# Performance work log

Hardware: AMD Instinct MI355X
Metric: run time of the kernel (lower is better)

The kernel has to match this reference:

```python
import jax, jax.numpy as jnp
import numpy as np

M_TOKENS = 8192
IN_F = 4096
OUT_F = 4096


def setup_inputs() -> dict:
    key = jax.random.key(0)
    k1, k2, k3, k4, k5 = jax.random.split(key, 5)
    x = jax.random.normal(k1, (M_TOKENS, IN_F), dtype=jnp.float32)
    # int8-range quantized weight, stored as int32 (values in [0, 255) like uint8 reinterpretation)
    w_q = jax.random.randint(k2, (OUT_F, IN_F), 0, 255, dtype=jnp.int32)
    scale = jax.random.uniform(k3, (OUT_F,), dtype=jnp.float32, minval=0.001, maxval=0.02)
    zero_point = jax.random.uniform(k4, (OUT_F,), dtype=jnp.float32, minval=0.0, maxval=128.0)
    bias = jax.random.normal(k5, (OUT_F,), dtype=jnp.float32)
    return {"x": x, "w_q": w_q, "scale": scale, "zero_point": zero_point, "bias": bias}


def reference(x, w_q, scale, zero_point, bias):
    # Per-channel (axis=0 / out_features) dequantization: w = (q - zp) * s
    w = (w_q.astype(jnp.float32) - zero_point[:, None]) * scale[:, None]  # [out, in]
    # F.linear: y = x @ w.T + b
    return jnp.einsum('mi,oi->mo', x, w) + bias
```

## Files before the change

### kernel.cpp

```cpp
#include <hip/hip_runtime.h>


typedef unsigned char u8;
typedef signed char s8;
typedef __attribute__((ext_vector_type(4))) int i32x4;
typedef __attribute__((ext_vector_type(4))) float f32x4;

#define M_TOK 8192
#define KDIM 4096
#define NDIM 4096
#define NT (KDIM / 128)


__device__ __forceinline__ int pack4(int a, int b, int c, int d) {
  return (a & 255) | ((b & 255) << 8) | ((c & 255) << 16) |
         (int)(((unsigned)(d & 255)) << 24);
}

#define GLDS(gptr, lptr)                                                      \
  __builtin_amdgcn_global_load_lds(                                          \
      (const __attribute__((address_space(1))) void*)(gptr),                 \
      (__attribute__((address_space(3))) void*)(lptr), 16, 0, 0)


__global__ __launch_bounds__(256) void convert_x_kernel(
    const float* __restrict__ x, s8* __restrict__ xq,
    float* __restrict__ sx, float* __restrict__ rq) {
  const int row = blockIdx.x;
  const int tid = threadIdx.x;
  const float* xr = x + (size_t)row * KDIM + tid * 16;
  float4 v[4];
#pragma unroll
  for (int i = 0; i < 4; ++i) v[i] = ((const float4*)xr)[i];

  float mx = 0.f;
#pragma unroll
  for (int i = 0; i < 4; ++i) {
    mx = fmaxf(mx, fabsf(v[i].x)); mx = fmaxf(mx, fabsf(v[i].y));
    mx = fmaxf(mx, fabsf(v[i].z)); mx = fmaxf(mx, fabsf(v[i].w));
  }
#pragma unroll
  for (int off = 32; off > 0; off >>= 1)
    mx = fmaxf(mx, __shfl_down(mx, off, 64));
  __shared__ float redf[4];
  __shared__ float bmax;
  if ((tid & 63) == 0) redf[tid >> 6] = mx;
  __syncthreads();
  if (tid == 0)
    bmax = fmaxf(fmaxf(redf[0], redf[1]), fmaxf(redf[2], redf[3]));
  __syncthreads();
  const float maxv = bmax;
  const float inv = 127.0f / fmaxf(maxv, 1e-30f);

  int q[16];
  int ssum = 0;
#pragma unroll
  for (int i = 0; i < 4; ++i) {
    q[i * 4 + 0] = (int)rintf(v[i].x * inv);
    q[i * 4 + 1] = (int)rintf(v[i].y * inv);
    q[i * 4 + 2] = (int)rintf(v[i].z * inv);
    q[i * 4 + 3] = (int)rintf(v[i].w * inv);
  }
#pragma unroll
  for (int i = 0; i < 16; ++i) ssum += q[i];

  int4 o;
  o.x = pack4(q[0], q[1], q[2], q[3]);
  o.y = pack4(q[4], q[5], q[6], q[7]);
  o.z = pack4(q[8], q[9], q[10], q[11]);
  o.w = pack4(q[12], q[13], q[14], q[15]);
  *(int4*)(xq + (size_t)row * KDIM + tid * 16) = o;

#pragma unroll
  for (int off = 32; off > 0; off >>= 1) ssum += __shfl_down(ssum, off, 64);
  __shared__ int redi[4];
  if ((tid & 63) == 0) redi[tid >> 6] = ssum;
  __syncthreads();
  if (tid == 0) {
    sx[row] = maxv * (1.0f / 127.0f);
    rq[row] = (float)(redi[0] + redi[1] + redi[2] + redi[3]);
  }
}


__global__ __launch_bounds__(256) void convert_w_kernel(
    const int* __restrict__ wq, s8* __restrict__ wb) {
  const size_t idx = (size_t)blockIdx.x * 256 + threadIdx.x;
  const int4* src = (const int4*)wq + idx * 4;
  const int4 a = src[0], b = src[1], c = src[2], d = src[3];
  int4 o;
  o.x = pack4(a.x - 128, a.y - 128, a.z - 128, a.w - 128);
  o.y = pack4(b.x - 128, b.y - 128, b.z - 128, b.w - 128);
  o.z = pack4(c.x - 128, c.y - 128, c.z - 128, c.w - 128);
  o.w = pack4(d.x - 128, d.y - 128, d.z - 128, d.w - 128);
  ((int4*)wb)[idx] = o;
}


__global__ __launch_bounds__(512, 2) void qlin_gemm_kernel(
    const u8* __restrict__ A,
    const u8* __restrict__ B,
    const float* __restrict__ sx,
    const float* __restrict__ rq,
    const float* __restrict__ scale,
    const float* __restrict__ zp,
    const float* __restrict__ bias,
    float* __restrict__ out) {
  extern __shared__ u8 lds[];
  u8* Al = lds;
  u8* Bl = lds + 65536;

  const int tid = threadIdx.x;
  const int lane = tid & 63;
  const int wave = tid >> 6;
  const int wm = wave >> 2;
  const int wn = wave & 3;

  const int bid = blockIdx.x;
  const int swz = (bid & 7) * 64 + (bid >> 3);
  const int bm = swz >> 4;
  const int bn = swz & 15;
  const int row0 = bm * 256, col0 = bn * 256;

  const int sr = tid >> 3;
  const int ss = (tid & 7) ^ (sr & 7);
  const u8* Ags = A + (size_t)(row0 + sr) * KDIM + ss * 16;
  const u8* Bgs = B + (size_t)(col0 + sr) * KDIM + ss * 16;
  u8* Ald = Al + wave * 1024;
  u8* Bld = Bl + wave * 1024;

#define STAGE_A(d, tau, h)                                                    \
  do {                                                                        \
    const u8* _g = Ags + (size_t)(h) * 128 * KDIM + (tau) * 128;             \
    u8* _l = Ald + (d) * 32768 + (h) * 16384;                                \
    GLDS(_g, _l);                                                            \
    GLDS(_g + (size_t)64 * KDIM, _l + 8192);                                 \
  } while (0)

#define STAGE_B(d, tau, h)                                                    \
  do {                                                                        \
    const u8* _g = Bgs + (size_t)(h) * 128 * KDIM + (tau) * 128;             \
    u8* _l = Bld + (d) * 32768 + (h) * 16384;                                \
    GLDS(_g, _l);                                                            \
    GLDS(_g + (size_t)64 * KDIM, _l + 8192);                                 \
  } while (0)

  const int r = lane & 15;
  const int g = lane >> 4;
  const int swzx = (lane & 7) << 4;
  const int ce0 = (g * 16) ^ swzx;
  const int ce1 = (64 + g * 16) ^ swzx;
  const u8* Ar = Al + (wm * 128 + r) * 128;
  const u8* Br = Bl + (wn * 64 + r) * 128;

#define LDA(base, m, ks) \
  (*(const i32x4*)((base) + (m) * 2048 + ((ks) ? ce1 : ce0)))
#define LDB(base, n, ks) \
  (*(const i32x4*)((base) + (n) * 2048 + ((ks) ? ce1 : ce0)))
#define MFMA(d, va, vb) \
  d = __builtin_amdgcn_mfma_i32_16x16x64_i8(va, vb, d, 0, 0, 0)

  i32x4 acc[8][4] = {};
  i32x4 a[8][2], b[4][2];

  STAGE_A(0, 0, 0); STAGE_A(0, 0, 1);
  STAGE_B(0, 0, 0); STAGE_B(0, 0, 1);
  STAGE_A(1, 1, 0); STAGE_A(1, 1, 1);
  asm volatile("s_waitcnt vmcnt(4)" ::: "memory");
  __builtin_amdgcn_s_barrier();
#pragma unroll
  for (int m = 0; m < 4; ++m) {
    a[m][0] = LDA(Ar, m, 0); a[m][1] = LDA(Ar, m, 1);
  }

  for (int t = 0; t < NT; ++t) {
    const int d = t & 1;
    const u8* Ard = Ar + d * 32768;
    const u8* Brd = Br + d * 32768;
    const u8* ArdN = Ar + (d ^ 1) * 32768;

#pragma unroll
    for (int n = 0; n < 2; ++n) {
      b[n][0] = LDB(Brd, n, 0); b[n][1] = LDB(Brd, n, 1);
    }
    asm volatile("" ::: "memory");
#pragma unroll
    for (int n = 2; n < 4; ++n) {
      b[n][0] = LDB(Brd, n, 0); b[n][1] = LDB(Brd, n, 1);
    }
    if (t + 1 < NT) STAGE_B(d ^ 1, t + 1, 0);
    __builtin_amdgcn_s_barrier();
    asm volatile("s_waitcnt lgkmcnt(4)" ::: "memory");
    __builtin_amdgcn_s_setprio(1);
#pragma unroll
    for (int m = 0; m < 4; ++m)
#pragma unroll
      for (int n = 0; n < 2; ++n) {
        MFMA(acc[m][n], a[m][0], b[n][0]);
        MFMA(acc[m][n], a[m][1], b[n][1]);
      }
    __builtin_amdgcn_s_setprio(0);
    __builtin_amdgcn_s_barrier();

#pragma unroll
    for (int m = 4; m < 8; ++m) {
      a[m][0] = LDA(Ard, m, 0); a[m][1] = LDA(Ard, m, 1);
    }
    if (t + 1 < NT) STAGE_B(d ^ 1, t + 1, 1);
    __builtin_amdgcn_s_barrier();
    asm volatile("s_waitcnt lgkmcnt(8)" ::: "memory");
    __builtin_amdgcn_s_setprio(1);
#pragma unroll
    for (int m = 0; m < 4; ++m)
#pragma unroll
      for (int n = 2; n < 4; ++n) {
        MFMA(acc[m][n], a[m][0], b[n][0]);
        MFMA(acc[m][n], a[m][1], b[n][1]);
      }
    __builtin_amdgcn_s_setprio(0);
    __builtin_amdgcn_s_barrier();

    if (t + 1 < NT) {
      asm volatile("s_waitcnt vmcnt(4)" ::: "memory");
    }
    __builtin_amdgcn_s_barrier();
    asm volatile("s_waitcnt lgkmcnt(0)" ::: "memory");
    __builtin_amdgcn_s_setprio(1);
#pragma unroll
    for (int m = 4; m < 8; ++m)
#pragma unroll
      for (int n = 0; n < 2; ++n) {
        MFMA(acc[m][n], a[m][0], b[n][0]);
        MFMA(acc[m][n], a[m][1], b[n][1]);
      }
    __builtin_amdgcn_s_setprio(0);
    __builtin_amdgcn_s_barrier();

    if (t + 1 < NT) {
#pragma unroll
      for (int m = 0; m < 4; ++m) {
        a[m][0] = LDA(ArdN, m, 0); a[m][1] = LDA(ArdN, m, 1);
      }
    }
    if (t + 2 < NT) { STAGE_A(d, t + 2, 0); STAGE_A(d, t + 2, 1); }
    __builtin_amdgcn_s_barrier();
    __builtin_amdgcn_s_setprio(1);
#pragma unroll
    for (int m = 4; m < 8; ++m)
#pragma unroll
      for (int n = 2; n < 4; ++n) {
        MFMA(acc[m][n], a[m][0], b[n][0]);
        MFMA(acc[m][n], a[m][1], b[n][1]);
      }
    __builtin_amdgcn_s_setprio(0);
    if (t < NT - 2) {
      asm volatile("s_waitcnt vmcnt(4)" ::: "memory");
    } else {
      asm volatile("s_waitcnt vmcnt(0)" ::: "memory");
    }
    __builtin_amdgcn_s_barrier();
  }

  {
    const int wrow0 = row0 + wm * 128;
    const int wcol0 = col0 + wn * 64;
    float* eps = (float*)lds + wave * 2176;
    const f32x4 p4 = *(const f32x4*)(scale + wcol0 + 4 * r);
    const f32x4 z4 = *(const f32x4*)(zp + wcol0 + 4 * r);
    const f32x4 b4 = *(const f32x4*)(bias + wcol0 + 4 * r);
    const f32x4 w04 = p4 * (128.0f - z4);
#pragma unroll
    for (int c = 0; c < 4; ++c) {
#pragma unroll
      for (int mm = 0; mm < 2; ++mm)
#pragma unroll
        for (int n = 0; n < 4; ++n)
#pragma unroll
          for (int q = 0; q < 4; ++q)
            eps[(mm * 16 + g * 4 + q) * 68 + n * 16 + r] =
                (float)acc[2 * c + mm][n][q];
      asm volatile("s_waitcnt lgkmcnt(0)" ::: "memory");
#pragma unroll
      for (int j = 0; j < 8; ++j) {
        const int rl = j * 4 + g;
        const int grow = wrow0 + c * 32 + rl;
        const f32x4 v = *(const f32x4*)(eps + rl * 68 + 4 * r);
        const float sxr = sx[grow];
        const float rqr = rq[grow];
        const f32x4 o4 = sxr * (p4 * v + w04 * rqr) + b4;
        *(f32x4*)(out + (size_t)grow * NDIM + wcol0 + 4 * r) = o4;
      }
      asm volatile("s_waitcnt lgkmcnt(0)" ::: "memory");
    }
  }
#undef STAGE_A
#undef STAGE_B
#undef LDA
#undef LDB
#undef MFMA
}


extern "C" void kernel_launch(void* const* d_in, const int* in_sizes, int n_in,
                              void* d_out, int out_size, void* d_ws,
                              size_t ws_size, hipStream_t stream) {
  const float* x = (const float*)d_in[0];
  const int* wq = (const int*)d_in[1];
  const float* scale = (const float*)d_in[2];
  const float* zp = (const float*)d_in[3];
  const float* bias = (const float*)d_in[4];
  float* out = (float*)d_out;

  char* ws = (char*)d_ws;
  s8* xq = (s8*)ws;
  s8* wq8 = (s8*)(ws + (size_t)M_TOK * KDIM);
  float* sx = (float*)(ws + (size_t)M_TOK * KDIM + (size_t)NDIM * KDIM);
  float* rq = (float*)(ws + (size_t)M_TOK * KDIM + (size_t)NDIM * KDIM +
                       (size_t)M_TOK * 4);

  (void)hipFuncSetAttribute((const void*)qlin_gemm_kernel,
                            hipFuncAttributeMaxDynamicSharedMemorySize,
                            131072);

  convert_x_kernel<<<M_TOK, 256, 0, stream>>>(x, xq, sx, rq);
  convert_w_kernel<<<(NDIM * (size_t)KDIM) / (256 * 16), 256, 0, stream>>>(
      wq, wq8);

  qlin_gemm_kernel<<<dim3((M_TOK / 256) * (NDIM / 256)), dim3(512), 131072,
                     stream>>>((const u8*)xq, (const u8*)wq8, sx, rq, scale,
                               zp, bias, out);
}
```

Baseline: 178.9 us.

## Halve K-tile to 64 and stage operands in MFMA fragment-native LDS layout

Shrinks the K-step per iteration from 128 to 64, halving LDS use from 128KB to 64KB, and changes the global-to-LDS staging so each lane writes its 16-byte MFMA fragment contiguously. LDS reads become linear per-lane accesses with no XOR swizzle. The epilogue staging buffer is resized and processes 16 rows per pass. The aim is cheaper bank-conflict-free LDS reads and possibly more residency, at the cost of twice as many iterations and barriers per output tile, each with half the MFMA work.

```diff
diff --git a/kernel.cpp b/kernel.cpp
--- a/kernel.cpp
+++ b/kernel.cpp
@@ -9,7 +9,7 @@
 #define M_TOK 8192
 #define KDIM 4096
 #define NDIM 4096
-#define NT (KDIM / 128)
+#define NT (KDIM / 64)
 
 
 __device__ __forceinline__ int pack4(int a, int b, int c, int d) {
@@ -108,7 +108,7 @@
     float* __restrict__ out) {
   extern __shared__ u8 lds[];
   u8* Al = lds;
-  u8* Bl = lds + 65536;
+  u8* Bl = lds + 32768;
 
   const int tid = threadIdx.x;
   const int lane = tid & 63;
@@ -122,106 +122,71 @@
   const int bn = swz & 15;
   const int row0 = bm * 256, col0 = bn * 256;
 
-  const int sr = tid >> 3;
-  const int ss = (tid & 7) ^ (sr & 7);
-  const u8* Ags = A + (size_t)(row0 + sr) * KDIM + ss * 16;
-  const u8* Bgs = B + (size_t)(col0 + sr) * KDIM + ss * 16;
-  u8* Ald = Al + wave * 1024;
-  u8* Bld = Bl + wave * 1024;
+  const int fr = lane & 15;
+  const int fk = lane >> 4;
+  const u8* Ags = A + (size_t)(row0 + wave * 16 + fr) * KDIM + fk * 16;
+  const u8* Bgs = B + (size_t)(col0 + wave * 16 + fr) * KDIM + fk * 16;
+  u8* AldW = Al + wave * 1024;
+  u8* BldW = Bl + wave * 1024;
 
 #define STAGE_A(d, tau, h)                                                    \
-  do {                                                                        \
-    const u8* _g = Ags + (size_t)(h) * 128 * KDIM + (tau) * 128;             \
-    u8* _l = Ald + (d) * 32768 + (h) * 16384;                                \
-    GLDS(_g, _l);                                                            \
-    GLDS(_g + (size_t)64 * KDIM, _l + 8192);                                 \
-  } while (0)
-
+  GLDS(Ags + (size_t)(h) * 128 * KDIM + (tau) * 64,                          \
+       AldW + (d) * 16384 + (h) * 8192)
 #define STAGE_B(d, tau, h)                                                    \
-  do {                                                                        \
-    const u8* _g = Bgs + (size_t)(h) * 128 * KDIM + (tau) * 128;             \
-    u8* _l = Bld + (d) * 32768 + (h) * 16384;                                \
-    GLDS(_g, _l);                                                            \
-    GLDS(_g + (size_t)64 * KDIM, _l + 8192);                                 \
-  } while (0)
-
-  const int r = lane & 15;
-  const int g = lane >> 4;
-  const int swzx = (lane & 7) << 4;
-  const int ce0 = (g * 16) ^ swzx;
-  const int ce1 = (64 + g * 16) ^ swzx;
-  const u8* Ar = Al + (wm * 128 + r) * 128;
-  const u8* Br = Bl + (wn * 64 + r) * 128;
-
-#define LDA(base, m, ks) \
-  (*(const i32x4*)((base) + (m) * 2048 + ((ks) ? ce1 : ce0)))
-#define LDB(base, n, ks) \
-  (*(const i32x4*)((base) + (n) * 2048 + ((ks) ? ce1 : ce0)))
+  GLDS(Bgs + (size_t)(h) * 128 * KDIM + (tau) * 64,                          \
+       BldW + (d) * 16384 + (h) * 8192)
+
+  const u8* ArL = Al + wm * 8192 + lane * 16;
+  const u8* BrL = Bl + (wn >> 1) * 8192 + (wn & 1) * 4096 + lane * 16;
+
+#define LDA(d, m) (*(const i32x4*)(ArL + (d) * 16384 + (m) * 1024))
+#define LDB(d, n) (*(const i32x4*)(BrL + (d) * 16384 + (n) * 1024))
 #define MFMA(d, va, vb) \
   d = __builtin_amdgcn_mfma_i32_16x16x64_i8(va, vb, d, 0, 0, 0)
 
   i32x4 acc[8][4] = {};
-  i32x4 a[8][2], b[4][2];
+  i32x4 a[8], b[4];
 
   STAGE_A(0, 0, 0); STAGE_A(0, 0, 1);
   STAGE_B(0, 0, 0); STAGE_B(0, 0, 1);
   STAGE_A(1, 1, 0); STAGE_A(1, 1, 1);
-  asm volatile("s_waitcnt vmcnt(4)" ::: "memory");
+  asm volatile("s_waitcnt vmcnt(2)" ::: "memory");
   __builtin_amdgcn_s_barrier();
 #pragma unroll
-  for (int m = 0; m < 4; ++m) {
-    a[m][0] = LDA(Ar, m, 0); a[m][1] = LDA(Ar, m, 1);
-  }
+  for (int m = 0; m < 4; ++m) a[m] = LDA(0, m);
 
   for (int t = 0; t < NT; ++t) {
     const int d = t & 1;
-    const u8* Ard = Ar + d * 32768;
-    const u8* Brd = Br + d * 32768;
-    const u8* ArdN = Ar + (d ^ 1) * 32768;
-
-#pragma unroll
-    for (int n = 0; n < 2; ++n) {
-      b[n][0] = LDB(Brd, n, 0); b[n][1] = LDB(Brd, n, 1);
-    }
+
+    b[0] = LDB(d, 0); b[1] = LDB(d, 1);
     asm volatile("" ::: "memory");
-#pragma unroll
-    for (int n = 2; n < 4; ++n) {
-      b[n][0] = LDB(Brd, n, 0); b[n][1] = LDB(Brd, n, 1);
-    }
+    b[2] = LDB(d, 2); b[3] = LDB(d, 3);
     if (t + 1 < NT) STAGE_B(d ^ 1, t + 1, 0);
     __builtin_amdgcn_s_barrier();
+    asm volatile("s_waitcnt lgkmcnt(2)" ::: "memory");
+    __builtin_amdgcn_s_setprio(1);
+#pragma unroll
+    for (int m = 0; m < 4; ++m)
+#pragma unroll
+      for (int n = 0; n < 2; ++n) MFMA(acc[m][n], a[m], b[n]);
+    __builtin_amdgcn_s_setprio(0);
+    __builtin_amdgcn_s_barrier();
+
+#pragma unroll
+    for (int m = 4; m < 8; ++m) a[m] = LDA(d, m);
+    if (t + 1 < NT) STAGE_B(d ^ 1, t + 1, 1);
+    __builtin_amdgcn_s_barrier();
     asm volatile("s_waitcnt lgkmcnt(4)" ::: "memory");
     __builtin_amdgcn_s_setprio(1);
 #pragma unroll
     for (int m = 0; m < 4; ++m)
 #pragma unroll
-      for (int n = 0; n < 2; ++n) {
-        MFMA(acc[m][n], a[m][0], b[n][0]);
-        MFMA(acc[m][n], a[m][1], b[n][1]);
-      }
-    __builtin_amdgcn_s_setprio(0);
-    __builtin_amdgcn_s_barrier();
-
-#pragma unroll
-    for (int m = 4; m < 8; ++m) {
-      a[m][0] = LDA(Ard, m, 0); a[m][1] = LDA(Ard, m, 1);
-    }
-    if (t + 1 < NT) STAGE_B(d ^ 1, t + 1, 1);
-    __builtin_amdgcn_s_barrier();
-    asm volatile("s_waitcnt lgkmcnt(8)" ::: "memory");
-    __builtin_amdgcn_s_setprio(1);
-#pragma unroll
-    for (int m = 0; m < 4; ++m)
-#pragma unroll
-      for (int n = 2; n < 4; ++n) {
-        MFMA(acc[m][n], a[m][0], b[n][0]);
-        MFMA(acc[m][n], a[m][1], b[n][1]);
-      }
+      for (int n = 2; n < 4; ++n) MFMA(acc[m][n], a[m], b[n]);
     __builtin_amdgcn_s_setprio(0);
     __builtin_amdgcn_s_barrier();
 
     if (t + 1 < NT) {
-      asm volatile("s_waitcnt vmcnt(4)" ::: "memory");
+      asm volatile("s_waitcnt vmcnt(2)" ::: "memory");
     }
     __builtin_amdgcn_s_barrier();
     asm volatile("s_waitcnt lgkmcnt(0)" ::: "memory");
@@ -229,18 +194,13 @@
 #pragma unroll
     for (int m = 4; m < 8; ++m)
 #pragma unroll
-      for (int n = 0; n < 2; ++n) {
-        MFMA(acc[m][n], a[m][0], b[n][0]);
-        MFMA(acc[m][n], a[m][1], b[n][1]);
-      }
+      for (int n = 0; n < 2; ++n) MFMA(acc[m][n], a[m], b[n]);
     __builtin_amdgcn_s_setprio(0);
     __builtin_amdgcn_s_barrier();
 
     if (t + 1 < NT) {
 #pragma unroll
-      for (int m = 0; m < 4; ++m) {
-        a[m][0] = LDA(ArdN, m, 0); a[m][1] = LDA(ArdN, m, 1);
-      }
+      for (int m = 0; m < 4; ++m) a[m] = LDA(d ^ 1, m);
     }
     if (t + 2 < NT) { STAGE_A(d, t + 2, 0); STAGE_A(d, t + 2, 1); }
     __builtin_amdgcn_s_barrier();
@@ -248,13 +208,10 @@
 #pragma unroll
     for (int m = 4; m < 8; ++m)
 #pragma unroll
-      for (int n = 2; n < 4; ++n) {
-        MFMA(acc[m][n], a[m][0], b[n][0]);
-        MFMA(acc[m][n], a[m][1], b[n][1]);
-      }
+      for (int n = 2; n < 4; ++n) MFMA(acc[m][n], a[m], b[n]);
     __builtin_amdgcn_s_setprio(0);
     if (t < NT - 2) {
-      asm volatile("s_waitcnt vmcnt(4)" ::: "memory");
+      asm volatile("s_waitcnt vmcnt(2)" ::: "memory");
     } else {
       asm volatile("s_waitcnt vmcnt(0)" ::: "memory");
     }
@@ -264,31 +221,28 @@
   {
     const int wrow0 = row0 + wm * 128;
     const int wcol0 = col0 + wn * 64;
-    float* eps = (float*)lds + wave * 2176;
-    const f32x4 p4 = *(const f32x4*)(scale + wcol0 + 4 * r);
-    const f32x4 z4 = *(const f32x4*)(zp + wcol0 + 4 * r);
-    const f32x4 b4 = *(const f32x4*)(bias + wcol0 + 4 * r);
+    float* eps = (float*)lds + wave * 1088;
+    const f32x4 p4 = *(const f32x4*)(scale + wcol0 + 4 * fr);
+    const f32x4 z4 = *(const f32x4*)(zp + wcol0 + 4 * fr);
+    const f32x4 b4 = *(const f32x4*)(bias + wcol0 + 4 * fr);
     const f32x4 w04 = p4 * (128.0f - z4);
 #pragma unroll
-    for (int c = 0; c < 4; ++c) {
-#pragma unroll
-      for (int mm = 0; mm < 2; ++mm)
-#pragma unroll
-        for (int n = 0; n < 4; ++n)
-#pragma unroll
-          for (int q = 0; q < 4; ++q)
-            eps[(mm * 16 + g * 4 + q) * 68 + n * 16 + r] =
-                (float)acc[2 * c + mm][n][q];
+    for (int c = 0; c < 8; ++c) {
+#pragma unroll
+      for (int n = 0; n < 4; ++n)
+#pragma unroll
+        for (int q = 0; q < 4; ++q)
+          eps[(fk * 4 + q) * 68 + n * 16 + fr] = (float)acc[c][n][q];
       asm volatile("s_waitcnt lgkmcnt(0)" ::: "memory");
 #pragma unroll
-      for (int j = 0; j < 8; ++j) {
-        const int rl = j * 4 + g;
-        const int grow = wrow0 + c * 32 + rl;
-        const f32x4 v = *(const f32x4*)(eps + rl * 68 + 4 * r);
+      for (int j = 0; j < 4; ++j) {
+        const int rl = j * 4 + fk;
+        const int grow = wrow0 + c * 16 + rl;
+        const f32x4 v = *(const f32x4*)(eps + rl * 68 + 4 * fr);
         const float sxr = sx[grow];
         const float rqr = rq[grow];
         const f32x4 o4 = sxr * (p4 * v + w04 * rqr) + b4;
-        *(f32x4*)(out + (size_t)grow * NDIM + wcol0 + 4 * r) = o4;
+        *(f32x4*)(out + (size_t)grow * NDIM + wcol0 + 4 * fr) = o4;
       }
       asm volatile("s_waitcnt lgkmcnt(0)" ::: "memory");
     }
@@ -320,13 +274,13 @@
 
   (void)hipFuncSetAttribute((const void*)qlin_gemm_kernel,
                             hipFuncAttributeMaxDynamicSharedMemorySize,
-                            131072);
+                            65536);
 
   convert_x_kernel<<<M_TOK, 256, 0, stream>>>(x, xq, sx, rq);
   convert_w_kernel<<<(NDIM * (size_t)KDIM) / (256 * 16), 256, 0, stream>>>(
       wq, wq8);
 
-  qlin_gemm_kernel<<<dim3((M_TOK / 256) * (NDIM / 256)), dim3(512), 131072,
+  qlin_gemm_kernel<<<dim3((M_TOK / 256) * (NDIM / 256)), dim3(512), 65536,
                      stream>>>((const u8*)xq, (const u8*)wq8, sx, rq, scale,
                                zp, bias, out);
 }
```

After: 198.1 us. 1.11x slower.

## Trim barriers and reorder MFMA k-steps in the main GEMM pipeline

Applied to the files above, without the earlier changes.

Removes several workgroup barriers from the four-phase inner loop. STAGE_A for tile t+2 moves earlier, right after an lgkmcnt(0) wait and a barrier, and the next-tile A LDS reads move after the vmcnt wait. MFMA loops are reordered so the k-step index is outermost, which spaces out dependent accumulations on the same accumulator. The aim is less barrier stall time and better overlap of global-to-LDS copies with MFMA work. The risk is LDS read/write hazards on the double buffer, since the ordering guarantees have changed.

```diff
diff --git a/kernel.cpp b/kernel.cpp
--- a/kernel.cpp
+++ b/kernel.cpp
@@ -193,14 +193,12 @@
     asm volatile("s_waitcnt lgkmcnt(4)" ::: "memory");
     __builtin_amdgcn_s_setprio(1);
 #pragma unroll
-    for (int m = 0; m < 4; ++m)
-#pragma unroll
-      for (int n = 0; n < 2; ++n) {
-        MFMA(acc[m][n], a[m][0], b[n][0]);
-        MFMA(acc[m][n], a[m][1], b[n][1]);
-      }
+    for (int ks = 0; ks < 2; ++ks)
+#pragma unroll
+      for (int m = 0; m < 4; ++m)
+#pragma unroll
+        for (int n = 0; n < 2; ++n) MFMA(acc[m][n], a[m][ks], b[n][ks]);
     __builtin_amdgcn_s_setprio(0);
-    __builtin_amdgcn_s_barrier();
 
 #pragma unroll
     for (int m = 4; m < 8; ++m) {
@@ -211,54 +209,45 @@
     asm volatile("s_waitcnt lgkmcnt(8)" ::: "memory");
     __builtin_amdgcn_s_setprio(1);
 #pragma unroll
-    for (int m = 0; m < 4; ++m)
-#pragma unroll
-      for (int n = 2; n < 4; ++n) {
-        MFMA(acc[m][n], a[m][0], b[n][0]);
-        MFMA(acc[m][n], a[m][1], b[n][1]);
-      }
+    for (int ks = 0; ks < 2; ++ks)
+#pragma unroll
+      for (int m = 0; m < 4; ++m)
+#pragma unroll
+        for (int n = 2; n < 4; ++n) MFMA(acc[m][n], a[m][ks], b[n][ks]);
     __builtin_amdgcn_s_setprio(0);
+
+    asm volatile("s_waitcnt lgkmcnt(0)" ::: "memory");
     __builtin_amdgcn_s_barrier();
-
-    if (t + 1 < NT) {
-      asm volatile("s_waitcnt vmcnt(4)" ::: "memory");
-    }
-    __builtin_amdgcn_s_barrier();
-    asm volatile("s_waitcnt lgkmcnt(0)" ::: "memory");
+    if (t + 2 < NT) { STAGE_A(d, t + 2, 0); STAGE_A(d, t + 2, 1); }
     __builtin_amdgcn_s_setprio(1);
 #pragma unroll
-    for (int m = 4; m < 8; ++m)
-#pragma unroll
-      for (int n = 0; n < 2; ++n) {
-        MFMA(acc[m][n], a[m][0], b[n][0]);
-        MFMA(acc[m][n], a[m][1], b[n][1]);
-      }
+    for (int ks = 0; ks < 2; ++ks)
+#pragma unroll
+      for (int m = 4; m < 8; ++m)
+#pragma unroll
+        for (int n = 0; n < 2; ++n) MFMA(acc[m][n], a[m][ks], b[n][ks]);
     __builtin_amdgcn_s_setprio(0);
-    __builtin_amdgcn_s_barrier();
-
-    if (t + 1 < NT) {
-#pragma unroll
-      for (int m = 0; m < 4; ++m) {
-        a[m][0] = LDA(ArdN, m, 0); a[m][1] = LDA(ArdN, m, 1);
-      }
-    }
-    if (t + 2 < NT) { STAGE_A(d, t + 2, 0); STAGE_A(d, t + 2, 1); }
-    __builtin_amdgcn_s_barrier();
-    __builtin_amdgcn_s_setprio(1);
-#pragma unroll
-    for (int m = 4; m < 8; ++m)
-#pragma unroll
-      for (int n = 2; n < 4; ++n) {
-        MFMA(acc[m][n], a[m][0], b[n][0]);
-        MFMA(acc[m][n], a[m][1], b[n][1]);
-      }
-    __builtin_amdgcn_s_setprio(0);
+
     if (t < NT - 2) {
       asm volatile("s_waitcnt vmcnt(4)" ::: "memory");
     } else {
       asm volatile("s_waitcnt vmcnt(0)" ::: "memory");
     }
     __builtin_amdgcn_s_barrier();
+    if (t + 1 < NT) {
+#pragma unroll
+      for (int m = 0; m < 4; ++m) {
+        a[m][0] = LDA(ArdN, m, 0); a[m][1] = LDA(ArdN, m, 1);
+      }
+    }
+    __builtin_amdgcn_s_setprio(1);
+#pragma unroll
+    for (int ks = 0; ks < 2; ++ks)
+#pragma unroll
+      for (int m = 4; m < 8; ++m)
+#pragma unroll
+        for (int n = 2; n < 4; ++n) MFMA(acc[m][n], a[m][ks], b[n][ks]);
+    __builtin_amdgcn_s_setprio(0);
   }
 
   {
```

Measured after the change: 172.8 us. 1.04x faster.
